# Kernel tuning notes

Measured on AMD Instinct MI355X. Metric: run time of the kernel, lower is better.

The kernel has to match this reference:

```python
import jax, jax.numpy as jnp
import numpy as np
from jax import lax

N, CIN, H, W = 32, 128, 64, 64
COUT, KH, KW = 256, 3, 3
STRIDE = (1, 1)
PADDING = ((1, 1), (1, 1))


def setup_inputs() -> dict:
    key = jax.random.key(0)
    k1, k2, k3, k4 = jax.random.split(key, 4)
    # binary input in {0,1}
    x = jax.random.randint(k1, (N, CIN, H, W), 0, 2).astype(jnp.float32)
    # ternary weight in {-1,0,1}
    weight = (jax.random.randint(k2, (COUT, CIN, KH, KW), 0, 3) - 1).astype(jnp.float32)
    # integer bias (folded from BN, floored to int per get_sign_bias_from_bn)
    bias = jax.random.randint(k3, (COUT,), -200, 200).astype(jnp.float32)
    # sign in {-1,+1}, broadcast shape (1, COUT, 1, 1)
    sign = jnp.where(jax.random.bernoulli(k4, 0.5, (1, COUT, 1, 1)), 1.0, -1.0).astype(jnp.float32)
    return {"x": x, "weight": weight, "bias": bias, "sign": sign}


def reference(x, weight, bias, sign):
    # y = conv2d(x, W) + bias  (stride 1, pad 1, NCHW)
    y = lax.conv_general_dilated(
        x, weight,
        window_strides=STRIDE,
        padding=PADDING,
        dimension_numbers=("NCHW", "OIHW", "NCHW"),
    ) + bias[None, :, None, None]
    # rounding=True -> torch.round_(y)
    y = jnp.round(y)
    # output = 1 iff sign * y >= 0, cast back to input dtype
    return jnp.where(y * sign >= 0, jnp.float32(1), jnp.float32(0)).astype(x.dtype)
```

## Files before the change

kernel.cpp:

```cpp
#include <hip/hip_runtime.h>
#include <cstdint>


#define NIMG 32
#define CIN  128
#define HH   64
#define WW   64
#define COUT 256
#define PH   66
#define XT_ROWSTRIDE (PH * CIN)
#define XT_NSTRIDE   (PH * PH * CIN)
#define XT_BYTES     ((size_t)NIMG * XT_NSTRIDE)
#define WP_TAPSTRIDE (COUT * CIN)
#define WP_BYTES     ((size_t)9 * WP_TAPSTRIDE)

typedef int v4i __attribute__((ext_vector_type(4)));

__global__ __launch_bounds__(256) void xt_prepass(const float* __restrict__ x,
                                                  int8_t* __restrict__ xt) {
    const int py = blockIdx.x;
    const int n  = blockIdx.y;
    const int t  = threadIdx.x;
    int8_t* rowbase = xt + (size_t)(n * PH + py) * XT_ROWSTRIDE;

    if (py == 0 || py == PH - 1) {
        int4 z = {0, 0, 0, 0};
        for (int j = t; j < XT_ROWSTRIDE / 16; j += 256)
            ((int4*)rowbase)[j] = z;
        return;
    }

    __shared__ __align__(16) int8_t Ls[64 * 144];
    const int y  = py - 1;
    const int xq = t & 15;
    const float4* xf = (const float4*)x;
#pragma unroll
    for (int j = 0; j < 8; ++j) {
        const int ci = (t >> 4) + j * 16;
        float4 v = xf[((size_t)(n * CIN + ci) * HH + y) * 16 + xq];
        const int xv = xq * 4;
        Ls[(xv + 0) * 144 + ci] = (int8_t)v.x;
        Ls[(xv + 1) * 144 + ci] = (int8_t)v.y;
        Ls[(xv + 2) * 144 + ci] = (int8_t)v.z;
        Ls[(xv + 3) * 144 + ci] = (int8_t)v.w;
    }
    __syncthreads();
    const int4 z = {0, 0, 0, 0};
    for (int j = t; j < XT_ROWSTRIDE / 16; j += 256) {
        const int px  = j >> 3;
        const int c   = j & 7;
        int4 val;
        if (px == 0 || px == PH - 1) val = z;
        else                         val = *(const int4*)&Ls[(px - 1) * 144 + c * 16];
        *(int4*)(rowbase + (size_t)px * CIN + ((c ^ (px & 7)) << 4)) = val;
    }
}

__global__ __launch_bounds__(256) void w_prepack(const float* __restrict__ w,
                                                 int8_t* __restrict__ wq) {
    const int idx = blockIdx.x * 256 + threadIdx.x;
    if (idx >= (int)WP_BYTES) return;
    const int tap = idx >> 15;
    const int rem = idx & 32767;
    const int co  = rem >> 7;
    const int ci  = rem & 127;
    const int half = ci >> 6, quad = (ci >> 4) & 3, b = ci & 15;
    const int cot = co >> 6, c = (co >> 4) & 3, row = co & 15;
    wq[tap * 32768 + cot * 8192 + half * 4096 + c * 1024
       + (quad * 16 + row) * 16 + b] =
        (int8_t)w[(size_t)(co * CIN + ci) * 9 + tap];
}

__device__ __forceinline__ void glds16(const void* g, uint32_t lds_off) {
    asm volatile("s_mov_b32 m0, %0\n"
                 "global_load_lds_dwordx4 %1, off"
                 :: "s"(lds_off), "v"(g) : "memory");
}

__global__ __launch_bounds__(256) void binconv_gemm(
    const int8_t* __restrict__ xt, const int8_t* __restrict__ wq,
    const float* __restrict__ bias, const float* __restrict__ sign,
    float* __restrict__ out) {

    __shared__ __align__(16) int8_t Xraw[4 * XT_ROWSTRIDE];

    const int t    = threadIdx.x;
    const int wid  = t >> 6;
    const int lane = t & 63;
    const int bx   = blockIdx.x;
    const int co0  = blockIdx.y * 128;
    const int n    = bx >> 5;
    const int y0   = (bx & 31) << 1;

    const int8_t* xbase = xt + (size_t)n * XT_NSTRIDE + (size_t)y0 * XT_ROWSTRIDE;
    {
        const int8_t* gsrc = xbase + lane * 16;
        const uint32_t lds0 = (uint32_t)(uintptr_t)Xraw;
        for (int j = wid; j < 33; j += 4)
            glds16(gsrc + j * 1024,
                   __builtin_amdgcn_readfirstlane(lds0 + j * 1024));
        asm volatile("s_waitcnt vmcnt(0)" ::: "memory");
        __syncthreads();
    }

    const int row    = lane & 15;
    const int quad   = lane >> 4;
    const int co_off = (wid >> 1) * 64;
    const int m_off  = (wid & 1) * 64;

    const int8_t* Xw  = Xraw + (wid & 1) * XT_ROWSTRIDE;
    const int8_t* wqb = wq + ((co0 + co_off) >> 6) * 8192 + lane * 16;

    v4i acc[4][4] = {};

#pragma unroll
    for (int tap = 0; tap < 9; ++tap) {
        const int ky = tap / 3, kx = tap % 3;
        const int8_t* wqt = wqb + tap * 32768;
        const int8_t* xl  = Xw + ky * XT_ROWSTRIDE;
        const int pxr = row + kx;

        v4i af[2][4];
#pragma unroll
        for (int h = 0; h < 2; ++h)
#pragma unroll
            for (int c = 0; c < 4; ++c)
                af[h][c] = *(const v4i*)(wqt + h * 4096 + c * 1024);

#pragma unroll
        for (int h = 0; h < 2; ++h) {
            const int swX = ((h * 4 + quad) ^ (pxr & 7)) << 4;
            v4i bf[4];
#pragma unroll
            for (int m = 0; m < 4; ++m)
                bf[m] = *(const v4i*)(xl + (pxr + m * 16) * CIN + swX);
#pragma unroll
            for (int c = 0; c < 4; ++c)
#pragma unroll
                for (int m = 0; m < 4; ++m)
                    acc[c][m] = __builtin_amdgcn_mfma_i32_16x16x64_i8(
                        af[h][c], bf[m], acc[c][m], 0, 0, 0);
        }
    }

    const float* bco = bias + co0 + co_off;
    const float* sco = sign + co0 + co_off;
    float* outb = out + ((size_t)n * COUT + co0 + co_off) * (HH * WW)
                + y0 * WW + m_off;
#pragma unroll
    for (int c = 0; c < 4; ++c) {
#pragma unroll
        for (int r = 0; r < 4; ++r) {
            const int col_co = c * 16 + quad * 4 + r;
            const float bv = bco[col_co];
            const float sv = sco[col_co];
            float* orow = outb + (size_t)col_co * (HH * WW);
#pragma unroll
            for (int m = 0; m < 4; ++m) {
                const float yv = (float)acc[c][m][r] + bv;
                const bool on = (sv > 0.0f) ? (yv >= 0.0f) : (yv <= 0.0f);
                orow[m * 16 + row] = on ? 1.0f : 0.0f;
            }
        }
    }
}

__global__ __launch_bounds__(256) void naive_conv(
    const float* __restrict__ x, const float* __restrict__ w,
    const float* __restrict__ bias, const float* __restrict__ sign,
    float* __restrict__ out) {
    const int idx = blockIdx.x * 256 + threadIdx.x;
    const int xc = idx & 63, y = (idx >> 6) & 63, co = (idx >> 12) & 255,
              n = idx >> 20;
    float s = 0.f;
    for (int ci = 0; ci < CIN; ++ci)
        for (int ky = 0; ky < 3; ++ky) {
            const int iy = y + ky - 1;
            if (iy < 0 || iy >= HH) continue;
            for (int kx = 0; kx < 3; ++kx) {
                const int ix = xc + kx - 1;
                if (ix < 0 || ix >= WW) continue;
                s += x[((size_t)(n * CIN + ci) * HH + iy) * WW + ix] *
                     w[((size_t)(co * CIN + ci) * 3 + ky) * 3 + kx];
            }
        }
    const float yv = s + bias[co];
    out[idx] = ((sign[co] > 0.f) ? (yv >= 0.f) : (yv <= 0.f)) ? 1.0f : 0.0f;
}

extern "C" void kernel_launch(void* const* d_in, const int* in_sizes, int n_in,
                              void* d_out, int out_size, void* d_ws, size_t ws_size,
                              hipStream_t stream) {
    const float* x    = (const float*)d_in[0];
    const float* w    = (const float*)d_in[1];
    const float* bias = (const float*)d_in[2];
    const float* sign = (const float*)d_in[3];
    float* out = (float*)d_out;

    const size_t need = XT_BYTES + WP_BYTES;
    if (ws_size < need) {
        naive_conv<<<dim3((NIMG * COUT * HH * WW) / 256), 256, 0, stream>>>(
            x, w, bias, sign, out);
        return;
    }
    int8_t* xt = (int8_t*)d_ws;
    int8_t* wq = (int8_t*)d_ws + XT_BYTES;

    xt_prepass<<<dim3(PH, NIMG), 256, 0, stream>>>(x, xt);
    w_prepack<<<dim3((int)(WP_BYTES + 255) / 256), 256, 0, stream>>>(w, wq);
    binconv_gemm<<<dim3(NIMG * (HH / 2), COUT / 128), 256, 0, stream>>>(
        xt, wq, bias, sign, out);
}
```

Measured before the change: 219.1 us.

## Switch int8 MFMA from 16x16x64 to 32x32x32 tiles with repacked weights

Replaces the 16x16x64 int8 MFMA tiling with 32x32x32 MFMA. Weights are repacked into a matching layout and the activation fragment loads are reorganised to use it. Each wave now holds 2x2 accumulators of 16 ints, and the epilogue applies bias and sign with integer arithmetic. The larger tile is meant to cut fragment loads per MFMA and LDS traffic. The cost is higher register pressure and different output store coalescing, and the integer epilogue assumes bias is integral.

```diff
diff --git a/kernel.cpp b/kernel.cpp
--- a/kernel.cpp
+++ b/kernel.cpp
@@ -14,7 +14,8 @@
 #define WP_TAPSTRIDE (COUT * CIN)
 #define WP_BYTES     ((size_t)9 * WP_TAPSTRIDE)
 
-typedef int v4i __attribute__((ext_vector_type(4)));
+typedef int   v4i  __attribute__((ext_vector_type(4)));
+typedef int   v16i __attribute__((ext_vector_type(16)));
 
 __global__ __launch_bounds__(256) void xt_prepass(const float* __restrict__ x,
                                                   int8_t* __restrict__ xt) {
@@ -64,10 +65,9 @@
     const int rem = idx & 32767;
     const int co  = rem >> 7;
     const int ci  = rem & 127;
-    const int half = ci >> 6, quad = (ci >> 4) & 3, b = ci & 15;
-    const int cot = co >> 6, c = (co >> 4) & 3, row = co & 15;
-    wq[tap * 32768 + cot * 8192 + half * 4096 + c * 1024
-       + (quad * 16 + row) * 16 + b] =
+    const int s = ci >> 5, hi = (ci >> 4) & 1, b = ci & 15;
+    const int co32 = co >> 5, lo = co & 31;
+    wq[(((tap * 8 + co32) * 4 + s) << 10) + ((hi * 32 + lo) << 4) + b] =
         (int8_t)w[(size_t)(co * CIN + ci) * 9 + tap];
 }
 
@@ -103,63 +103,67 @@
         __syncthreads();
     }
 
-    const int row    = lane & 15;
-    const int quad   = lane >> 4;
+    const int m_lo = lane & 31;
+    const int hi   = lane >> 5;
     const int co_off = (wid >> 1) * 64;
-    const int m_off  = (wid & 1) * 64;
-
-    const int8_t* Xw  = Xraw + (wid & 1) * XT_ROWSTRIDE;
-    const int8_t* wqb = wq + ((co0 + co_off) >> 6) * 8192 + lane * 16;
-
-    v4i acc[4][4] = {};
+    const int yw     = wid & 1;
+    const int ct0  = (co0 + co_off) >> 5;
+
+    const int8_t* Xw  = Xraw + yw * XT_ROWSTRIDE;
+    const int8_t* wqb = wq + lane * 16;
+
+    v16i acc[2][2] = {};
 
 #pragma unroll
     for (int tap = 0; tap < 9; ++tap) {
         const int ky = tap / 3, kx = tap % 3;
-        const int8_t* wqt = wqb + tap * 32768;
-        const int8_t* xl  = Xw + ky * XT_ROWSTRIDE;
-        const int pxr = row + kx;
+        const int8_t* xl = Xw + ky * XT_ROWSTRIDE;
+        const int px0 = m_lo + kx;
+        const int pk  = px0 & 7;
 
         v4i af[2][4];
 #pragma unroll
-        for (int h = 0; h < 2; ++h)
-#pragma unroll
-            for (int c = 0; c < 4; ++c)
-                af[h][c] = *(const v4i*)(wqt + h * 4096 + c * 1024);
-
-#pragma unroll
-        for (int h = 0; h < 2; ++h) {
-            const int swX = ((h * 4 + quad) ^ (pxr & 7)) << 4;
-            v4i bf[4];
-#pragma unroll
-            for (int m = 0; m < 4; ++m)
-                bf[m] = *(const v4i*)(xl + (pxr + m * 16) * CIN + swX);
-#pragma unroll
-            for (int c = 0; c < 4; ++c)
-#pragma unroll
-                for (int m = 0; m < 4; ++m)
-                    acc[c][m] = __builtin_amdgcn_mfma_i32_16x16x64_i8(
-                        af[h][c], bf[m], acc[c][m], 0, 0, 0);
+        for (int c = 0; c < 2; ++c)
+#pragma unroll
+            for (int s = 0; s < 4; ++s)
+                af[c][s] = *(const v4i*)(wqb
+                    + ((((tap * 8 + ct0 + c) * 4) + s) << 10));
+
+        const int8_t* xb = xl + px0 * CIN;
+        v4i bf[2][4];
+#pragma unroll
+        for (int s = 0; s < 4; ++s) {
+            const int sw = ((2 * s + hi) ^ pk) << 4;
+#pragma unroll
+            for (int m = 0; m < 2; ++m)
+                bf[m][s] = *(const v4i*)(xb + m * 32 * CIN + sw);
         }
+#pragma unroll
+        for (int s = 0; s < 4; ++s)
+#pragma unroll
+            for (int c = 0; c < 2; ++c)
+#pragma unroll
+                for (int m = 0; m < 2; ++m)
+                    acc[c][m] = __builtin_amdgcn_mfma_i32_32x32x32_i8(
+                        af[c][s], bf[m][s], acc[c][m], 0, 0, 0);
     }
 
     const float* bco = bias + co0 + co_off;
     const float* sco = sign + co0 + co_off;
     float* outb = out + ((size_t)n * COUT + co0 + co_off) * (HH * WW)
-                + y0 * WW + m_off;
-#pragma unroll
-    for (int c = 0; c < 4; ++c) {
-#pragma unroll
-        for (int r = 0; r < 4; ++r) {
-            const int col_co = c * 16 + quad * 4 + r;
-            const float bv = bco[col_co];
-            const float sv = sco[col_co];
-            float* orow = outb + (size_t)col_co * (HH * WW);
-#pragma unroll
-            for (int m = 0; m < 4; ++m) {
-                const float yv = (float)acc[c][m][r] + bv;
-                const bool on = (sv > 0.0f) ? (yv >= 0.0f) : (yv <= 0.0f);
-                orow[m * 16 + row] = on ? 1.0f : 0.0f;
+                + (y0 + yw) * WW;
+#pragma unroll
+    for (int c = 0; c < 2; ++c) {
+#pragma unroll
+        for (int r = 0; r < 16; ++r) {
+            const int co_l = c * 32 + (r & 3) + 8 * (r >> 2) + 4 * hi;
+            const int bi = (int)bco[co_l];
+            const int si = (int)sco[co_l];
+            float* orow = outb + (size_t)co_l * (HH * WW);
+#pragma unroll
+            for (int m = 0; m < 2; ++m) {
+                const int tv = (acc[c][m][r] + bi) * si;
+                orow[m * 32 + m_lo] = (tv >= 0) ? 1.0f : 0.0f;
             }
         }
     }
```

Result: slower. 228.3 us (+4.2%).
